# Kernel optimization log

Hardware: AMD Instinct MI355X
Metric: run time of the kernel (lower is better)

The kernel has to match this reference:

```python
import jax, jax.numpy as jnp
import numpy as np

B, T, C = 2, 1024, 2048
H, N = 32, 64
D_DECAY = 96; D_AAA = 96; D_MV = 64; D_GATE = 256
EPS_GN = 1e-5 * 64.0  # eps * head_size_divisor**2, divisor=8


def setup_inputs() -> dict:
    key = jax.random.key(0)
    ks = jax.random.split(key, 24)
    rn = lambda k, s, sc=1.0: jax.random.normal(k, s, jnp.float32) * sc
    ru = lambda k, s: jax.random.uniform(k, s, jnp.float32)
    sw = C ** -0.5
    return dict(
        x=rn(ks[0], (B, T, C)),
        v_first=rn(ks[1], (B, T, C)),
        shift_state=rn(ks[2], (B, C)),
        wkv_state=jnp.zeros((B, H, N, N), jnp.float32),
        x_r=ru(ks[3], (1, 1, C)), x_w=ru(ks[4], (1, 1, C)), x_k=ru(ks[5], (1, 1, C)),
        x_v=ru(ks[6], (1, 1, C)), x_a=ru(ks[7], (1, 1, C)), x_g=ru(ks[8], (1, 1, C)),
        w0=jnp.linspace(-7.0, -2.0, C, dtype=jnp.float32).reshape(1, 1, C) + 0.5,
        w1=rn(ks[9], (C, D_DECAY), sw), w2=rn(ks[10], (D_DECAY, C), 0.1 * D_DECAY ** -0.5),
        a0=jnp.zeros((1, 1, C), jnp.float32),
        a1=rn(ks[11], (C, D_AAA), sw), a2=rn(ks[12], (D_AAA, C), 0.1 * D_AAA ** -0.5),
        v0=jnp.ones((1, 1, C), jnp.float32),
        v1=rn(ks[13], (C, D_MV), sw), v2=rn(ks[14], (D_MV, C), 0.1 * D_MV ** -0.5),
        g1=rn(ks[15], (C, D_GATE), sw), g2=rn(ks[16], (D_GATE, C), 0.1 * D_GATE ** -0.5),
        k_k=0.85 * jnp.ones((1, 1, C), jnp.float32),
        k_a=jnp.ones((1, 1, C), jnp.float32),
        r_k=rn(ks[17], (H, N), 0.1),
        W_r=rn(ks[18], (C, C), sw), W_k=rn(ks[19], (C, C), sw),
        W_v=rn(ks[20], (C, C), sw), W_o=rn(ks[21], (C, C), sw),
        gn_w=jnp.ones((C,), jnp.float32), gn_b=jnp.zeros((C,), jnp.float32),
    )


def _forward(x, v_first, shift_state, wkv_state, x_r, x_w, x_k, x_v, x_a, x_g,
             w0, w1, w2, a0, a1, a2, v0, v1, v2, g1, g2, k_k, k_a, r_k,
             W_r, W_k, W_v, W_o, gn_w, gn_b):
    # token shift (ZeroPad2d((0,0,1,-1)) == prepend shift_state, drop last)
    xx = jnp.concatenate([shift_state[:, None, :], x[:, :-1]], axis=1) - x
    xr = x + xx * x_r; xw = x + xx * x_w; xk = x + xx * x_k
    xv = x + xx * x_v; xa = x + xx * x_a; xg = x + xx * x_g
    r = xr @ W_r.T
    w = -jax.nn.softplus(-(w0 + jnp.tanh(xw @ w1) @ w2)) - 0.5  # <= -0.5
    k = xk @ W_k.T
    v = xv @ W_v.T
    v = v + (v_first - v) * jax.nn.sigmoid(v0 + (xv @ v1) @ v2)  # layer_id != 0
    a = jax.nn.sigmoid(a0 + (xa @ a1) @ a2)
    g = jax.nn.sigmoid(xg @ g1) @ g2
    kk = (k * k_k).reshape(B, T, H, N)
    kk = kk / jnp.maximum(jnp.linalg.norm(kk, axis=-1, keepdims=True), 1e-12)  # F.normalize
    k = k * (1.0 + (a - 1.0) * k_a)
    # RWKV-7 recurrence: S_t = S * diag(exp(-exp(w))) + (S a) b^T + v k^T ; o_t = S r
    wdec = jnp.exp(-jnp.exp(w))                           # [B,T,C] in (0,1)
    tm = lambda z: z.reshape(B, T, H, N).transpose(1, 0, 2, 3)  # -> [T,B,H,N]
    xs = (tm(r), tm(wdec), tm(k), tm(v),
          -kk.transpose(1, 0, 2, 3),
          (kk * a.reshape(B, T, H, N)).transpose(1, 0, 2, 3))

    def step(S, ins):  # S: [B,H,N_v,N_k]
        rr, ww, kc, vv, aa, bb = ins
        Sa = jnp.einsum('bhvk,bhk->bhv', S, aa)
        S = S * ww[:, :, None, :] + Sa[..., None] * bb[:, :, None, :] + vv[..., None] * kc[:, :, None, :]
        return S, jnp.einsum('bhvk,bhk->bhv', S, rr)

    S_f, o = jax.lax.scan(step, wkv_state, xs)
    o = o.transpose(1, 0, 2, 3)                           # [B,T,H,N]
    # GroupNorm(H, C): per-(B*T) sample, normalize each head's N channels
    mu = o.mean(-1, keepdims=True)
    var = o.var(-1, keepdims=True)
    o = (o - mu) * jax.lax.rsqrt(var + EPS_GN) * gn_w.reshape(H, N) + gn_b.reshape(H, N)
    rh = r.reshape(B, T, H, N); kh = k.reshape(B, T, H, N); vh = v.reshape(B, T, H, N)
    o = o + (rh * kh * r_k).sum(-1, keepdims=True) * vh
    out = (o.reshape(B, T, C) * g) @ W_o.T
    return out, S_f


def reference(x, v_first, shift_state, wkv_state, x_r, x_w, x_k, x_v, x_a, x_g,
              w0, w1, w2, a0, a1, a2, v0, v1, v2, g1, g2, k_k, k_a, r_k,
              W_r, W_k, W_v, W_o, gn_w, gn_b):
    out, S_f = _forward(x, v_first, shift_state, wkv_state, x_r, x_w, x_k, x_v, x_a, x_g,
                        w0, w1, w2, a0, a1, a2, v0, v1, v2, g1, g2, k_k, k_a, r_k,
                        W_r, W_k, W_v, W_o, gn_w, gn_b)
    return (out, S_f)
```

## Files before the change

### kernel.cpp

```cpp
#include <hip/hip_runtime.h>
#include <stdint.h>

typedef __attribute__((ext_vector_type(4))) float f32x4;
typedef __attribute__((ext_vector_type(8))) __bf16 bf16x8;

#define DEVINL __device__ __forceinline__

constexpr int T_LEN = 1024;
constexpr int CDIM  = 2048;
constexpr int MROWS = 2048;
constexpr size_t MC = (size_t)MROWS * CDIM;

constexpr size_t SZ_BF  = MC * 2;
constexpr size_t SZ_F32 = MC * 4;
constexpr size_t oXr  = 0;
constexpr size_t oXw  = oXr + SZ_BF;
constexpr size_t oXk  = oXw + SZ_BF;
constexpr size_t oXv  = oXk + SZ_BF;
constexpr size_t oXa  = oXv + SZ_BF;
constexpr size_t oXg  = oXa + SZ_BF;
constexpr size_t oWr  = oXg + SZ_BF;
constexpr size_t oWk  = oWr + SZ_BF;
constexpr size_t oWv  = oWk + SZ_BF;
constexpr size_t oWo  = oWv + SZ_BF;
constexpr size_t oW1T = oWo + SZ_BF;
constexpr size_t oA1T = oW1T + 524288;
constexpr size_t oV1T = oA1T + 524288;
constexpr size_t oG1T = oV1T + 524288;
constexpr size_t oW2T = oG1T + 1048576;
constexpr size_t oA2T = oW2T + 524288;
constexpr size_t oV2T = oA2T + 524288;
constexpr size_t oG2T = oV2T + 524288;
constexpr size_t oHw  = oG2T + 1048576;
constexpr size_t oHa  = oHw + 524288;
constexpr size_t oHv  = oHa + 524288;
constexpr size_t oHg  = oHv + 524288;
constexpr size_t oR   = oHg + 1048576;
constexpr size_t oK   = oR  + SZ_F32;
constexpr size_t oV   = oK  + SZ_F32;
constexpr size_t oWW  = oV  + SZ_F32;
constexpr size_t oAA  = oWW + SZ_F32;
constexpr size_t oBB  = oAA + SZ_F32;
constexpr size_t oG   = oBB + SZ_F32;
constexpr size_t oO   = oG  + SZ_F32;
constexpr size_t oAout= oO  + SZ_F32;

DEVINL unsigned short f2bf(float f) {
  uint32_t u = __builtin_bit_cast(uint32_t, f);
  u += 0x7fffu + ((u >> 16) & 1u);
  return (unsigned short)(u >> 16);
}
DEVINL void st_bf4(unsigned short* p, f32x4 v) {
  ushort4 o;
  o.x = f2bf(v[0]); o.y = f2bf(v[1]); o.z = f2bf(v[2]); o.w = f2bf(v[3]);
  *(ushort4*)p = o;
}
DEVINL void gload16(const void* g, void* l) {
  __builtin_amdgcn_global_load_lds(
      (const __attribute__((address_space(1))) unsigned int*)g,
      (__attribute__((address_space(3))) unsigned int*)l, 16, 0, 0);
}

__global__ void k_conv_bf16(const float* __restrict__ s, unsigned short* __restrict__ d, int n4) {
  int i = blockIdx.x * 256 + threadIdx.x;
  if (i >= n4) return;
  f32x4 v = *(const f32x4*)(s + (size_t)i * 4);
  st_bf4(d + (size_t)i * 4, v);
}

struct TpJobs {
  const float* src[8];
  unsigned short* dst[8];
  int sR[8]; int sC[8]; int dR[8]; int dC[8];
};
__global__ void k_tp8(TpJobs jt) {
  const int j = blockIdx.y;
  const int n = jt.dR[j] * jt.dC[j];
  int i = blockIdx.x * 256 + threadIdx.x;
  if (i >= n) return;
  const int dC = jt.dC[j], sR = jt.sR[j], sC = jt.sC[j];
  int r = i / dC, c = i - r * dC;
  float v = (r < sC && c < sR) ? jt.src[j][(size_t)c * sC + r] : 0.f;
  jt.dst[j][i] = f2bf(v);
}

__global__ void k_mix(const float* __restrict__ x, const float* __restrict__ shift,
                      const float* __restrict__ cr, const float* __restrict__ cw,
                      const float* __restrict__ ck, const float* __restrict__ cv,
                      const float* __restrict__ ca, const float* __restrict__ cg,
                      unsigned short* __restrict__ Xr, unsigned short* __restrict__ Xw,
                      unsigned short* __restrict__ Xk, unsigned short* __restrict__ Xv,
                      unsigned short* __restrict__ Xa, unsigned short* __restrict__ Xg) {
  int i = blockIdx.x * 256 + threadIdx.x;
  size_t e = (size_t)i * 4;
  int m = (int)(e >> 11);
  int c = (int)(e & 2047);
  int t = m & (T_LEN - 1);
  int b = m >> 10;
  f32x4 xc = *(const f32x4*)(x + e);
  f32x4 pv = (t == 0) ? *(const f32x4*)(shift + (size_t)b * CDIM + c)
                      : *(const f32x4*)(x + e - CDIM);
  f32x4 xx = pv - xc;
  st_bf4(Xr + e, xc + xx * (*(const f32x4*)(cr + c)));
  st_bf4(Xw + e, xc + xx * (*(const f32x4*)(cw + c)));
  st_bf4(Xk + e, xc + xx * (*(const f32x4*)(ck + c)));
  st_bf4(Xv + e, xc + xx * (*(const f32x4*)(cv + c)));
  st_bf4(Xa + e, xc + xx * (*(const f32x4*)(ca + c)));
  st_bf4(Xg + e, xc + xx * (*(const f32x4*)(cg + c)));
}

struct GemmJob { const unsigned short* A; const unsigned short* B; void* C; int epi; };
struct GemmBatch { GemmJob j[3]; };

__global__ __launch_bounds__(256) void k_gemm_nt(GemmBatch gb, int K, int ldc) {
  const GemmJob jb = gb.j[blockIdx.z];
  __shared__ __align__(16) unsigned short As[128 * 32];
  __shared__ __align__(16) unsigned short Bs[128 * 32];
  const int tid  = threadIdx.x;
  const int lane = tid & 63;
  const int wv   = tid >> 6;
  const int wm = wv >> 1, wn = wv & 1;
  const int rowB = blockIdx.y * 128;
  const int colB = blockIdx.x * 128;
  const size_t rsb = (size_t)K * 2;
  const int c0 = wv, c1 = wv + 4;
  const char* Ag0 = (const char*)jb.A + (size_t)(rowB + c0 * 16 + (lane >> 2)) * rsb + (lane & 3) * 16;
  const char* Ag1 = (const char*)jb.A + (size_t)(rowB + c1 * 16 + (lane >> 2)) * rsb + (lane & 3) * 16;
  const char* Bg0 = (const char*)jb.B + (size_t)(colB + c0 * 16 + (lane >> 2)) * rsb + (lane & 3) * 16;
  const char* Bg1 = (const char*)jb.B + (size_t)(colB + c1 * 16 + (lane >> 2)) * rsb + (lane & 3) * 16;
  unsigned short* Al0 = As + c0 * 512;
  unsigned short* Al1 = As + c1 * 512;
  unsigned short* Bl0 = Bs + c0 * 512;
  unsigned short* Bl1 = Bs + c1 * 512;
  f32x4 acc[4][4];
#pragma unroll
  for (int mi = 0; mi < 4; ++mi)
#pragma unroll
    for (int ni = 0; ni < 4; ++ni) acc[mi][ni] = (f32x4){0.f, 0.f, 0.f, 0.f};
  const int KT = K >> 5;
  const int fr = lane & 15, fk = (lane >> 4) * 8;
  for (int kt = 0; kt < KT; ++kt) {
    __syncthreads();
    gload16(Ag0, Al0); gload16(Ag1, Al1);
    gload16(Bg0, Bl0); gload16(Bg1, Bl1);
    Ag0 += 64; Ag1 += 64; Bg0 += 64; Bg1 += 64;
    __syncthreads();
    bf16x8 af[4], bfv[4];
#pragma unroll
    for (int mi = 0; mi < 4; ++mi)
      af[mi] = *(const bf16x8*)&As[(wm * 64 + mi * 16 + fr) * 32 + fk];
#pragma unroll
    for (int ni = 0; ni < 4; ++ni)
      bfv[ni] = *(const bf16x8*)&Bs[(wn * 64 + ni * 16 + fr) * 32 + fk];
#pragma unroll
    for (int mi = 0; mi < 4; ++mi)
#pragma unroll
      for (int ni = 0; ni < 4; ++ni)
        acc[mi][ni] = __builtin_amdgcn_mfma_f32_16x16x32_bf16(af[mi], bfv[ni], acc[mi][ni], 0, 0, 0);
  }
  const int er = (lane >> 4) * 4, ec = lane & 15;
  if (jb.epi == 0) {
    float* Cf = (float*)jb.C;
#pragma unroll
    for (int mi = 0; mi < 4; ++mi)
#pragma unroll
      for (int ni = 0; ni < 4; ++ni) {
        int row0 = rowB + wm * 64 + mi * 16 + er;
        int col  = colB + wn * 64 + ni * 16 + ec;
#pragma unroll
        for (int j = 0; j < 4; ++j)
          Cf[(size_t)(row0 + j) * ldc + col] = acc[mi][ni][j];
      }
  } else {
    unsigned short* Cb = (unsigned short*)jb.C;
#pragma unroll
    for (int mi = 0; mi < 4; ++mi)
#pragma unroll
      for (int ni = 0; ni < 4; ++ni) {
        int row0 = rowB + wm * 64 + mi * 16 + er;
        int col  = colB + wn * 64 + ni * 16 + ec;
#pragma unroll
        for (int j = 0; j < 4; ++j) {
          float val = acc[mi][ni][j];
          if (jb.epi == 2) val = tanhf(val);
          else if (jb.epi == 3) val = 1.f / (1.f + __expf(-val));
          Cb[(size_t)(row0 + j) * ldc + col] = f2bf(val);
        }
      }
  }
}

__global__ __launch_bounds__(256) void k_post(
    float* __restrict__ Kb, float* __restrict__ Vb, float* __restrict__ Wb,
    float* __restrict__ Ab, float* __restrict__ Bb,
    const float* __restrict__ vf, const float* __restrict__ w0,
    const float* __restrict__ a0, const float* __restrict__ v0,
    const float* __restrict__ kkc, const float* __restrict__ kac) {
  int gw = blockIdx.x * 4 + (threadIdx.x >> 6);
  int lane = threadIdx.x & 63;
  int m = gw >> 5, h = gw & 31;
  int c = h * 64 + lane;
  size_t idx = (size_t)m * CDIM + c;
  float kraw = Kb[idx], vraw = Vb[idx], wlr = Wb[idx], alr = Ab[idx], vlr = Bb[idx];
  float z = w0[c] + wlr;
  float sg = 1.f / (1.f + __expf(-z));
  float wdec = __expf(-0.60653065971f * sg);
  float a = 1.f / (1.f + __expf(-(a0[c] + alr)));
  float vgate = 1.f / (1.f + __expf(-(v0[c] + vlr)));
  float v = vraw + (vf[idx] - vraw) * vgate;
  float kk = kraw * kkc[c];
  float s2 = kk * kk;
#pragma unroll
  for (int off = 32; off; off >>= 1) s2 += __shfl_xor(s2, off);
  float inv = 1.f / fmaxf(sqrtf(s2), 1e-12f);
  kk *= inv;
  float kn = kraw * (1.f + (a - 1.f) * kac[c]);
  Wb[idx] = wdec; Vb[idx] = v; Kb[idx] = kn; Ab[idx] = -kk; Bb[idx] = kk * a;
}

__global__ __launch_bounds__(64) void k_scan(
    const float* __restrict__ Rb, const float* __restrict__ Wb,
    const float* __restrict__ Kb, const float* __restrict__ Vb,
    const float* __restrict__ Ab, const float* __restrict__ Bb,
    const float* __restrict__ S0, float* __restrict__ Ob,
    float* __restrict__ Sf) {
  const int bid = blockIdx.x;
  const int bh = bid & 63, vo = bid >> 6;
  const int b = bh >> 5, h = bh & 31;
  const int lane = threadIdx.x;
  const int vr = lane & 7;
  const int kq = lane >> 3;
  const int gv = vo * 8 + vr;
  const int kk0 = kq * 8;
  __shared__ __align__(16) float stg[4][6][64];
  const size_t rowBase = (size_t)b * T_LEN * CDIM;
  const size_t colBase = (size_t)h * 64;
  const float* pR = Rb + rowBase + colBase + lane;
  const float* pW = Wb + rowBase + colBase + lane;
  const float* pK = Kb + rowBase + colBase + lane;
  const float* pV = Vb + rowBase + colBase + lane;
  const float* pA = Ab + rowBase + colBase + lane;
  const float* pB = Bb + rowBase + colBase + lane;
  float* Obp = Ob + rowBase + colBase + vo * 8 + lane;
  f32x4 s0, s1;
  {
    const float* sp = S0 + (((size_t)(b * 32 + h)) * 64 + gv) * 64 + kk0;
    s0 = *(const f32x4*)sp; s1 = *(const f32x4*)(sp + 4);
  }
  float gA[6], gB[6];
  {
    float h0[6], h1[6];
    h0[0] = pR[0]; h0[1] = pW[0]; h0[2] = pK[0]; h0[3] = pV[0]; h0[4] = pA[0]; h0[5] = pB[0];
    h1[0] = pR[CDIM]; h1[1] = pW[CDIM]; h1[2] = pK[CDIM]; h1[3] = pV[CDIM]; h1[4] = pA[CDIM]; h1[5] = pB[CDIM];
#pragma unroll
    for (int j = 0; j < 6; ++j) { stg[0][j][lane] = h0[j]; stg[1][j][lane] = h1[j]; }
    gA[0] = pR[2 * CDIM]; gA[1] = pW[2 * CDIM]; gA[2] = pK[2 * CDIM];
    gA[3] = pV[2 * CDIM]; gA[4] = pA[2 * CDIM]; gA[5] = pB[2 * CDIM];
    gB[0] = pR[3 * CDIM]; gB[1] = pW[3 * CDIM]; gB[2] = pK[3 * CDIM];
    gB[3] = pV[3 * CDIM]; gB[4] = pA[3 * CDIM]; gB[5] = pB[3 * CDIM];
  }
  f32x4 aR0, aR1, aW0, aW1, aK0, aK1, aA0, aA1, aB0, aB1; float aVV;
  f32x4 bR0, bR1, bW0, bW1, bK0, bK1, bA0, bA1, bB0, bB1; float bVV;
  aR0 = *(const f32x4*)&stg[0][0][kk0]; aR1 = *(const f32x4*)&stg[0][0][kk0 + 4];
  aW0 = *(const f32x4*)&stg[0][1][kk0]; aW1 = *(const f32x4*)&stg[0][1][kk0 + 4];
  aK0 = *(const f32x4*)&stg[0][2][kk0]; aK1 = *(const f32x4*)&stg[0][2][kk0 + 4];
  aA0 = *(const f32x4*)&stg[0][4][kk0]; aA1 = *(const f32x4*)&stg[0][4][kk0 + 4];
  aB0 = *(const f32x4*)&stg[0][5][kk0]; aB1 = *(const f32x4*)&stg[0][5][kk0 + 4];
  aVV = stg[0][3][gv];
  float pox = 0.f;
#define SCAN_STEP(T, G, SR0,SR1,SW0,SW1,SK0,SK1,SA0,SA1,SB0,SB1,SVV,           \
                  NR0,NR1,NW0,NW1,NK0,NK1,NA0,NA1,NB0,NB1,NVV, FIRST) do {     \
    f32x4 _sv = SA0 * s0 + SA1 * s1;                                           \
    float _sa = _sv[0] + _sv[1] + _sv[2] + _sv[3];                             \
    { const int _np = ((T) + 1) & 3;          \
      NR0 = *(const f32x4*)&stg[_np][0][kk0]; NR1 = *(const f32x4*)&stg[_np][0][kk0 + 4]; \
      NW0 = *(const f32x4*)&stg[_np][1][kk0]; NW1 = *(const f32x4*)&stg[_np][1][kk0 + 4]; \
      NK0 = *(const f32x4*)&stg[_np][2][kk0]; NK1 = *(const f32x4*)&stg[_np][2][kk0 + 4]; \
      NA0 = *(const f32x4*)&stg[_np][4][kk0]; NA1 = *(const f32x4*)&stg[_np][4][kk0 + 4]; \
      NB0 = *(const f32x4*)&stg[_np][5][kk0]; NB1 = *(const f32x4*)&stg[_np][5][kk0 + 4]; \
      NVV = stg[_np][3][gv]; }                                                 \
    float _po = pox;                                                           \
    _sa += __shfl_xor(_sa, 8);  _po += __shfl_xor(_po, 8);                     \
    _sa += __shfl_xor(_sa, 16); _po += __shfl_xor(_po, 16);                    \
    _sa += __shfl_xor(_sa, 32); _po += __shfl_xor(_po, 32);                    \
    if (!(FIRST) && lane < 8) Obp[(size_t)((T) - 1) * CDIM] = _po;             \
    { const int _ws = ((T) + 2) & 3;                                           \
      stg[_ws][0][lane] = G[0]; stg[_ws][1][lane] = G[1];                      \
      stg[_ws][2][lane] = G[2]; stg[_ws][3][lane] = G[3];                      \
      stg[_ws][4][lane] = G[4]; stg[_ws][5][lane] = G[5];                      \
      const size_t _to = (size_t)(((T) + 4 < T_LEN) ? (T) + 4 : T_LEN - 1) * CDIM; \
      G[0] = pR[_to]; G[1] = pW[_to]; G[2] = pK[_to];                          \
      G[3] = pV[_to]; G[4] = pA[_to]; G[5] = pB[_to]; }                        \
    s0 = s0 * SW0 + _sa * SB0 + SVV * SK0;                                     \
    s1 = s1 * SW1 + _sa * SB1 + SVV * SK1;                                     \
    f32x4 _ov = s0 * SR0 + s1 * SR1;                                           \
    pox = _ov[0] + _ov[1] + _ov[2] + _ov[3];                                   \
  } while (0)
#define SCAN_STEP_I(...) SCAN_STEP(__VA_ARGS__)
#define ASET aR0,aR1,aW0,aW1,aK0,aK1,aA0,aA1,aB0,aB1,aVV
#define BSET bR0,bR1,bW0,bW1,bK0,bK1,bA0,bA1,bB0,bB1,bVV
  SCAN_STEP_I(0, gA, ASET, BSET, true);
  SCAN_STEP_I(1, gB, BSET, ASET, false);
  for (int t = 2; t < T_LEN; t += 2) {
    SCAN_STEP_I(t, gA, ASET, BSET, false);
    SCAN_STEP_I(t + 1, gB, BSET, ASET, false);
  }
#undef SCAN_STEP
#undef SCAN_STEP_I
#undef ASET
#undef BSET
  {
    float _po = pox;
    _po += __shfl_xor(_po, 8);
    _po += __shfl_xor(_po, 16);
    _po += __shfl_xor(_po, 32);
    if (lane < 8) Obp[(size_t)(T_LEN - 1) * CDIM] = _po;
  }
  float* sfp = Sf + (((size_t)(b * 32 + h)) * 64 + gv) * 64 + kk0;
  *(f32x4*)sfp = s0; *(f32x4*)(sfp + 4) = s1;
}

__global__ __launch_bounds__(256) void k_gn(
    const float* __restrict__ Ob, const float* __restrict__ Rb,
    const float* __restrict__ Kb, const float* __restrict__ Vb,
    const float* __restrict__ Gb, const float* __restrict__ rk,
    const float* __restrict__ gw, const float* __restrict__ gb2,
    unsigned short* __restrict__ Aout) {
  int gwv = blockIdx.x * 4 + (threadIdx.x >> 6);
  int lane = threadIdx.x & 63;
  int m = gwv >> 5, h = gwv & 31;
  int c = h * 64 + lane;
  size_t idx = (size_t)m * CDIM + c;
  float o = Ob[idx], r = Rb[idx], k = Kb[idx], v = Vb[idx], g = Gb[idx];
  float t1 = o, t2 = o * o, t3 = r * k * rk[c];
#pragma unroll
  for (int off = 32; off; off >>= 1) {
    t1 += __shfl_xor(t1, off);
    t2 += __shfl_xor(t2, off);
    t3 += __shfl_xor(t3, off);
  }
  float mean = t1 * (1.f / 64.f);
  float var = t2 * (1.f / 64.f) - mean * mean;
  float og = (o - mean) * rsqrtf(var + 6.4e-4f) * gw[c] + gb2[c];
  og += t3 * v;
  Aout[idx] = f2bf(og * g);
}

extern "C" void kernel_launch(void* const* d_in, const int* in_sizes, int n_in,
                              void* d_out, int out_size, void* d_ws, size_t ws_size,
                              hipStream_t stream) {
  (void)in_sizes; (void)n_in; (void)out_size; (void)ws_size;
  const float* x      = (const float*)d_in[0];
  const float* vfirst = (const float*)d_in[1];
  const float* shift  = (const float*)d_in[2];
  const float* wkv0   = (const float*)d_in[3];
  const float* xr_c   = (const float*)d_in[4];
  const float* xw_c   = (const float*)d_in[5];
  const float* xk_c   = (const float*)d_in[6];
  const float* xv_c   = (const float*)d_in[7];
  const float* xa_c   = (const float*)d_in[8];
  const float* xg_c   = (const float*)d_in[9];
  const float* w0     = (const float*)d_in[10];
  const float* w1     = (const float*)d_in[11];
  const float* w2     = (const float*)d_in[12];
  const float* a0     = (const float*)d_in[13];
  const float* a1     = (const float*)d_in[14];
  const float* a2     = (const float*)d_in[15];
  const float* v0     = (const float*)d_in[16];
  const float* v1     = (const float*)d_in[17];
  const float* v2     = (const float*)d_in[18];
  const float* g1     = (const float*)d_in[19];
  const float* g2     = (const float*)d_in[20];
  const float* k_k    = (const float*)d_in[21];
  const float* k_a    = (const float*)d_in[22];
  const float* r_k    = (const float*)d_in[23];
  const float* W_r    = (const float*)d_in[24];
  const float* W_k    = (const float*)d_in[25];
  const float* W_v    = (const float*)d_in[26];
  const float* W_o    = (const float*)d_in[27];
  const float* gn_w   = (const float*)d_in[28];
  const float* gn_b   = (const float*)d_in[29];
  char* ws = (char*)d_ws;
  auto BF = [&](size_t o) { return (unsigned short*)(ws + o); };
  auto FP = [&](size_t o) { return (float*)(ws + o); };

  k_conv_bf16<<<4096, 256, 0, stream>>>(W_r, BF(oWr), 1048576);
  k_conv_bf16<<<4096, 256, 0, stream>>>(W_k, BF(oWk), 1048576);
  k_conv_bf16<<<4096, 256, 0, stream>>>(W_v, BF(oWv), 1048576);
  k_conv_bf16<<<4096, 256, 0, stream>>>(W_o, BF(oWo), 1048576);
  { TpJobs jt{};
    jt.src[0] = w1; jt.dst[0] = BF(oW1T); jt.sR[0] = 2048; jt.sC[0] = 96;   jt.dR[0] = 128;  jt.dC[0] = 2048;
    jt.src[1] = a1; jt.dst[1] = BF(oA1T); jt.sR[1] = 2048; jt.sC[1] = 96;   jt.dR[1] = 128;  jt.dC[1] = 2048;
    jt.src[2] = v1; jt.dst[2] = BF(oV1T); jt.sR[2] = 2048; jt.sC[2] = 64;   jt.dR[2] = 128;  jt.dC[2] = 2048;
    jt.src[3] = g1; jt.dst[3] = BF(oG1T); jt.sR[3] = 2048; jt.sC[3] = 256;  jt.dR[3] = 256;  jt.dC[3] = 2048;
    jt.src[4] = w2; jt.dst[4] = BF(oW2T); jt.sR[4] = 96;   jt.sC[4] = 2048; jt.dR[4] = 2048; jt.dC[4] = 128;
    jt.src[5] = a2; jt.dst[5] = BF(oA2T); jt.sR[5] = 96;   jt.sC[5] = 2048; jt.dR[5] = 2048; jt.dC[5] = 128;
    jt.src[6] = v2; jt.dst[6] = BF(oV2T); jt.sR[6] = 64;   jt.sC[6] = 2048; jt.dR[6] = 2048; jt.dC[6] = 128;
    jt.src[7] = g2; jt.dst[7] = BF(oG2T); jt.sR[7] = 256;  jt.sC[7] = 2048; jt.dR[7] = 2048; jt.dC[7] = 256;
    k_tp8<<<dim3(2048, 8), 256, 0, stream>>>(jt); }
  k_mix<<<4096, 256, 0, stream>>>(x, shift, xr_c, xw_c, xk_c, xv_c, xa_c, xg_c,
                                  BF(oXr), BF(oXw), BF(oXk), BF(oXv), BF(oXa), BF(oXg));
  { GemmBatch gb{};
    gb.j[0] = {BF(oXr), BF(oWr), FP(oR), 0};
    gb.j[1] = {BF(oXk), BF(oWk), FP(oK), 0};
    gb.j[2] = {BF(oXv), BF(oWv), FP(oV), 0};
    k_gemm_nt<<<dim3(16, 16, 3), 256, 0, stream>>>(gb, 2048, 2048); }
  { GemmBatch gb{};
    gb.j[0] = {BF(oXw), BF(oW1T), BF(oHw), 2};
    gb.j[1] = {BF(oXa), BF(oA1T), BF(oHa), 1};
    gb.j[2] = {BF(oXv), BF(oV1T), BF(oHv), 1};
    k_gemm_nt<<<dim3(1, 16, 3), 256, 0, stream>>>(gb, 2048, 128); }
  { GemmBatch gb{};
    gb.j[0] = {BF(oXg), BF(oG1T), BF(oHg), 3};
    k_gemm_nt<<<dim3(2, 16, 1), 256, 0, stream>>>(gb, 2048, 256); }
  { GemmBatch gb{};
    gb.j[0] = {BF(oHw), BF(oW2T), FP(oWW), 0};
    gb.j[1] = {BF(oHa), BF(oA2T), FP(oAA), 0};
    gb.j[2] = {BF(oHv), BF(oV2T), FP(oBB), 0};
    k_gemm_nt<<<dim3(16, 16, 3), 256, 0, stream>>>(gb, 128, 2048); }
  { GemmBatch gb{};
    gb.j[0] = {BF(oHg), BF(oG2T), FP(oG), 0};
    k_gemm_nt<<<dim3(16, 16, 1), 256, 0, stream>>>(gb, 256, 2048); }
  k_post<<<16384, 256, 0, stream>>>(FP(oK), FP(oV), FP(oWW), FP(oAA), FP(oBB),
                                    vfirst, w0, a0, v0, k_k, k_a);
  k_scan<<<512, 64, 0, stream>>>(FP(oR), FP(oWW), FP(oK), FP(oV), FP(oAA), FP(oBB),
                                 wkv0, FP(oO), (float*)d_out + MC);
  k_gn<<<16384, 256, 0, stream>>>(FP(oO), FP(oR), FP(oK), FP(oV), FP(oG),
                                  r_k, gn_w, gn_b, BF(oAout));
  { GemmBatch gb{};
    gb.j[0] = {BF(oAout), BF(oWo), d_out, 0};
    k_gemm_nt<<<dim3(16, 16, 1), 256, 0, stream>>>(gb, 2048, 2048); }
}
```

Before: 651.3 us.

## Widen per-lane state slice in WKV scan to 16 keys, halve scan blocks

The recurrent scan kernel now gives each lane a 16-element slice of the state row (16 value rows by 4 key quarters per block) instead of 8, so the grid drops from 512 to 256 wavefronts. This removes one shuffle stage from each of the two per-step reductions and halves redundant staging and global loading of the shared per-timestep vectors. The double-buffered register prefetch of the next step's operands is replaced by loading them from shared memory inside the step, with only the 'a' vector prefetched. The trade is fewer wavefronts, and so less latency hiding across the GPU, plus more serial FMA work per lane on the sequential critical path.

```diff
diff --git a/kernel.cpp b/kernel.cpp
--- a/kernel.cpp
+++ b/kernel.cpp
@@ -228,10 +228,10 @@
   const int bh = bid & 63, vo = bid >> 6;
   const int b = bh >> 5, h = bh & 31;
   const int lane = threadIdx.x;
-  const int vr = lane & 7;
-  const int kq = lane >> 3;
-  const int gv = vo * 8 + vr;
-  const int kk0 = kq * 8;
+  const int vr = lane & 15;
+  const int kq = lane >> 4;
+  const int gv = vo * 16 + vr;
+  const int kk0 = kq * 16;
   __shared__ __align__(16) float stg[4][6][64];
   const size_t rowBase = (size_t)b * T_LEN * CDIM;
   const size_t colBase = (size_t)h * 64;
@@ -241,11 +241,12 @@
   const float* pV = Vb + rowBase + colBase + lane;
   const float* pA = Ab + rowBase + colBase + lane;
   const float* pB = Bb + rowBase + colBase + lane;
-  float* Obp = Ob + rowBase + colBase + vo * 8 + lane;
-  f32x4 s0, s1;
+  float* Obp = Ob + rowBase + colBase + vo * 16 + lane;
+  f32x4 s0, s1, s2, s3;
   {
     const float* sp = S0 + (((size_t)(b * 32 + h)) * 64 + gv) * 64 + kk0;
-    s0 = *(const f32x4*)sp; s1 = *(const f32x4*)(sp + 4);
+    s0 = *(const f32x4*)sp;       s1 = *(const f32x4*)(sp + 4);
+    s2 = *(const f32x4*)(sp + 8); s3 = *(const f32x4*)(sp + 12);
   }
   float gA[6], gB[6];
   {
@@ -259,31 +260,43 @@
     gB[0] = pR[3 * CDIM]; gB[1] = pW[3 * CDIM]; gB[2] = pK[3 * CDIM];
     gB[3] = pV[3 * CDIM]; gB[4] = pA[3 * CDIM]; gB[5] = pB[3 * CDIM];
   }
-  f32x4 aR0, aR1, aW0, aW1, aK0, aK1, aA0, aA1, aB0, aB1; float aVV;
-  f32x4 bR0, bR1, bW0, bW1, bK0, bK1, bA0, bA1, bB0, bB1; float bVV;
-  aR0 = *(const f32x4*)&stg[0][0][kk0]; aR1 = *(const f32x4*)&stg[0][0][kk0 + 4];
-  aW0 = *(const f32x4*)&stg[0][1][kk0]; aW1 = *(const f32x4*)&stg[0][1][kk0 + 4];
-  aK0 = *(const f32x4*)&stg[0][2][kk0]; aK1 = *(const f32x4*)&stg[0][2][kk0 + 4];
-  aA0 = *(const f32x4*)&stg[0][4][kk0]; aA1 = *(const f32x4*)&stg[0][4][kk0 + 4];
-  aB0 = *(const f32x4*)&stg[0][5][kk0]; aB1 = *(const f32x4*)&stg[0][5][kk0 + 4];
-  aVV = stg[0][3][gv];
+  f32x4 nA0 = *(const f32x4*)&stg[0][4][kk0];
+  f32x4 nA1 = *(const f32x4*)&stg[0][4][kk0 + 4];
+  f32x4 nA2 = *(const f32x4*)&stg[0][4][kk0 + 8];
+  f32x4 nA3 = *(const f32x4*)&stg[0][4][kk0 + 12];
   float pox = 0.f;
-#define SCAN_STEP(T, G, SR0,SR1,SW0,SW1,SK0,SK1,SA0,SA1,SB0,SB1,SVV,           \
-                  NR0,NR1,NW0,NW1,NK0,NK1,NA0,NA1,NB0,NB1,NVV, FIRST) do {     \
-    f32x4 _sv = SA0 * s0 + SA1 * s1;                                           \
+#define SCAN_STEP(T, G, FIRST) do {                                            \
+    const int _sl = (T) & 3;                                                   \
+    f32x4 _sva = nA0 * s0 + nA1 * s1;                                          \
+    f32x4 _svb = nA2 * s2 + nA3 * s3;                                          \
+    f32x4 _sv = _sva + _svb;                                                   \
     float _sa = _sv[0] + _sv[1] + _sv[2] + _sv[3];                             \
-    { const int _np = ((T) + 1) & 3;          \
-      NR0 = *(const f32x4*)&stg[_np][0][kk0]; NR1 = *(const f32x4*)&stg[_np][0][kk0 + 4]; \
-      NW0 = *(const f32x4*)&stg[_np][1][kk0]; NW1 = *(const f32x4*)&stg[_np][1][kk0 + 4]; \
-      NK0 = *(const f32x4*)&stg[_np][2][kk0]; NK1 = *(const f32x4*)&stg[_np][2][kk0 + 4]; \
-      NA0 = *(const f32x4*)&stg[_np][4][kk0]; NA1 = *(const f32x4*)&stg[_np][4][kk0 + 4]; \
-      NB0 = *(const f32x4*)&stg[_np][5][kk0]; NB1 = *(const f32x4*)&stg[_np][5][kk0 + 4]; \
-      NVV = stg[_np][3][gv]; }                                                 \
     float _po = pox;                                                           \
-    _sa += __shfl_xor(_sa, 8);  _po += __shfl_xor(_po, 8);                     \
     _sa += __shfl_xor(_sa, 16); _po += __shfl_xor(_po, 16);                    \
     _sa += __shfl_xor(_sa, 32); _po += __shfl_xor(_po, 32);                    \
-    if (!(FIRST) && lane < 8) Obp[(size_t)((T) - 1) * CDIM] = _po;             \
+    const f32x4 _w0 = *(const f32x4*)&stg[_sl][1][kk0];                        \
+    const f32x4 _w1 = *(const f32x4*)&stg[_sl][1][kk0 + 4];                    \
+    const f32x4 _w2 = *(const f32x4*)&stg[_sl][1][kk0 + 8];                    \
+    const f32x4 _w3 = *(const f32x4*)&stg[_sl][1][kk0 + 12];                   \
+    const f32x4 _k0 = *(const f32x4*)&stg[_sl][2][kk0];                        \
+    const f32x4 _k1 = *(const f32x4*)&stg[_sl][2][kk0 + 4];                    \
+    const f32x4 _k2 = *(const f32x4*)&stg[_sl][2][kk0 + 8];                    \
+    const f32x4 _k3 = *(const f32x4*)&stg[_sl][2][kk0 + 12];                   \
+    const f32x4 _b0 = *(const f32x4*)&stg[_sl][5][kk0];                        \
+    const f32x4 _b1 = *(const f32x4*)&stg[_sl][5][kk0 + 4];                    \
+    const f32x4 _b2 = *(const f32x4*)&stg[_sl][5][kk0 + 8];                    \
+    const f32x4 _b3 = *(const f32x4*)&stg[_sl][5][kk0 + 12];                   \
+    const float _vv = stg[_sl][3][gv];                                         \
+    const f32x4 _r0 = *(const f32x4*)&stg[_sl][0][kk0];                        \
+    const f32x4 _r1 = *(const f32x4*)&stg[_sl][0][kk0 + 4];                    \
+    const f32x4 _r2 = *(const f32x4*)&stg[_sl][0][kk0 + 8];                    \
+    const f32x4 _r3 = *(const f32x4*)&stg[_sl][0][kk0 + 12];                   \
+    { const int _np = ((T) + 1) & 3;                 \
+      nA0 = *(const f32x4*)&stg[_np][4][kk0];                                  \
+      nA1 = *(const f32x4*)&stg[_np][4][kk0 + 4];                              \
+      nA2 = *(const f32x4*)&stg[_np][4][kk0 + 8];                              \
+      nA3 = *(const f32x4*)&stg[_np][4][kk0 + 12]; }                           \
+    if (!(FIRST) && lane < 16) Obp[(size_t)((T) - 1) * CDIM] = _po;            \
     { const int _ws = ((T) + 2) & 3;                                           \
       stg[_ws][0][lane] = G[0]; stg[_ws][1][lane] = G[1];                      \
       stg[_ws][2][lane] = G[2]; stg[_ws][3][lane] = G[3];                      \
@@ -291,33 +304,31 @@
       const size_t _to = (size_t)(((T) + 4 < T_LEN) ? (T) + 4 : T_LEN - 1) * CDIM; \
       G[0] = pR[_to]; G[1] = pW[_to]; G[2] = pK[_to];                          \
       G[3] = pV[_to]; G[4] = pA[_to]; G[5] = pB[_to]; }                        \
-    s0 = s0 * SW0 + _sa * SB0 + SVV * SK0;                                     \
-    s1 = s1 * SW1 + _sa * SB1 + SVV * SK1;                                     \
-    f32x4 _ov = s0 * SR0 + s1 * SR1;                                           \
+    s0 = s0 * _w0 + _sa * _b0 + _vv * _k0;                                     \
+    s1 = s1 * _w1 + _sa * _b1 + _vv * _k1;                                     \
+    s2 = s2 * _w2 + _sa * _b2 + _vv * _k2;                                     \
+    s3 = s3 * _w3 + _sa * _b3 + _vv * _k3;                                     \
+    f32x4 _ova = s0 * _r0 + s1 * _r1;                                          \
+    f32x4 _ovb = s2 * _r2 + s3 * _r3;                                          \
+    f32x4 _ov = _ova + _ovb;                                                   \
     pox = _ov[0] + _ov[1] + _ov[2] + _ov[3];                                   \
   } while (0)
-#define SCAN_STEP_I(...) SCAN_STEP(__VA_ARGS__)
-#define ASET aR0,aR1,aW0,aW1,aK0,aK1,aA0,aA1,aB0,aB1,aVV
-#define BSET bR0,bR1,bW0,bW1,bK0,bK1,bA0,bA1,bB0,bB1,bVV
-  SCAN_STEP_I(0, gA, ASET, BSET, true);
-  SCAN_STEP_I(1, gB, BSET, ASET, false);
+  SCAN_STEP(0, gA, true);
+  SCAN_STEP(1, gB, false);
   for (int t = 2; t < T_LEN; t += 2) {
-    SCAN_STEP_I(t, gA, ASET, BSET, false);
-    SCAN_STEP_I(t + 1, gB, BSET, ASET, false);
+    SCAN_STEP(t, gA, false);
+    SCAN_STEP(t + 1, gB, false);
   }
 #undef SCAN_STEP
-#undef SCAN_STEP_I
-#undef ASET
-#undef BSET
   {
     float _po = pox;
-    _po += __shfl_xor(_po, 8);
     _po += __shfl_xor(_po, 16);
     _po += __shfl_xor(_po, 32);
-    if (lane < 8) Obp[(size_t)(T_LEN - 1) * CDIM] = _po;
+    if (lane < 16) Obp[(size_t)(T_LEN - 1) * CDIM] = _po;
   }
   float* sfp = Sf + (((size_t)(b * 32 + h)) * 64 + gv) * 64 + kk0;
   *(f32x4*)sfp = s0; *(f32x4*)(sfp + 4) = s1;
+  *(f32x4*)(sfp + 8) = s2; *(f32x4*)(sfp + 12) = s3;
 }
 
 __global__ __launch_bounds__(256) void k_gn(
@@ -423,7 +434,7 @@
     k_gemm_nt<<<dim3(16, 16, 1), 256, 0, stream>>>(gb, 256, 2048); }
   k_post<<<16384, 256, 0, stream>>>(FP(oK), FP(oV), FP(oWW), FP(oAA), FP(oBB),
                                     vfirst, w0, a0, v0, k_k, k_a);
-  k_scan<<<512, 64, 0, stream>>>(FP(oR), FP(oWW), FP(oK), FP(oV), FP(oAA), FP(oBB),
+  k_scan<<<256, 64, 0, stream>>>(FP(oR), FP(oWW), FP(oK), FP(oV), FP(oAA), FP(oBB),
                                  wkv0, FP(oO), (float*)d_out + MC);
   k_gn<<<16384, 256, 0, stream>>>(FP(oO), FP(oR), FP(oK), FP(oV), FP(oG),
                                   r_k, gn_w, gn_b, BF(oAout));
```

After: 693.6 us. 1.06x slower.
